# Kernel optimization log

Measured on AMD Instinct MI355X. Metric: run time of the kernel, lower is better.

## Reference

```python
import jax, jax.numpy as jnp
import numpy as np

NUM_SLOTS = 8
DIM = 256
N_HEADS = 4
ITERS = 5
HIDDEN = 512
EPS = 1e-8
DPH = DIM // N_HEADS
SCALE = DPH ** -0.5


def _ln(x, g, b):
    mu = x.mean(-1, keepdims=True)
    var = ((x - mu) ** 2).mean(-1, keepdims=True)
    return (x - mu) * jax.lax.rsqrt(var + 1e-5) * g + b


def setup_inputs() -> dict:
    key = jax.random.key(0)
    ks = jax.random.split(key, 12)
    B, N = 32, 4096
    def p(k, shape, s=0.02):
        return jax.random.normal(k, shape, jnp.float32) * s
    return {
        'inputs': jax.random.normal(ks[0], (B, N, DIM), jnp.float32),
        'slots_init': jax.random.normal(ks[1], (B, NUM_SLOTS, DIM), jnp.float32),
        'ln_f_g': jnp.ones(DIM, jnp.float32), 'ln_f_b': jnp.zeros(DIM, jnp.float32),
        'ln_s_g': jnp.ones(DIM, jnp.float32), 'ln_s_b': jnp.zeros(DIM, jnp.float32),
        'ln_ff_g': jnp.ones(DIM, jnp.float32), 'ln_ff_b': jnp.zeros(DIM, jnp.float32),
        'Wq': p(ks[2], (DIM, DIM)), 'bq': jnp.zeros(DIM, jnp.float32),
        'Wk': p(ks[3], (DIM, DIM)), 'bk': jnp.zeros(DIM, jnp.float32),
        'Wv': p(ks[4], (DIM, DIM)), 'bv': jnp.zeros(DIM, jnp.float32),
        'W_ih': p(ks[5], (3 * DIM, DIM)), 'b_ih': jnp.zeros(3 * DIM, jnp.float32),
        'W_hh': p(ks[6], (3 * DIM, DIM)), 'b_hh': jnp.zeros(3 * DIM, jnp.float32),
        'W1': p(ks[7], (DIM, HIDDEN)), 'b1': jnp.zeros(HIDDEN, jnp.float32),
        'W2': p(ks[8], (HIDDEN, DIM)), 'b2': jnp.zeros(DIM, jnp.float32),
    }


def reference(inputs, slots_init, ln_f_g, ln_f_b, ln_s_g, ln_s_b, ln_ff_g, ln_ff_b,
              Wq, bq, Wk, bk, Wv, bv, W_ih, b_ih, W_hh, b_hh, W1, b1, W2, b2):
    b, n, d = inputs.shape
    ns = slots_init.shape[1]
    x = _ln(inputs, ln_f_g, ln_f_b)                      # [b,n,d]
    k = (x @ Wk + bk).reshape(b, n, N_HEADS, DPH)
    v = (x @ Wv + bv).reshape(b, n, N_HEADS, DPH)
    slots = slots_init
    for _ in range(ITERS):
        slots_prev = slots
        s = _ln(slots, ln_s_g, ln_s_b)
        q = (s @ Wq + bq).reshape(b, ns, N_HEADS, DPH)
        dots = jnp.einsum('bihd,bjhd->bihj', q, k) * SCALE   # [b,ns,h,n]
        # softmax jointly over (slots, heads) per feature location j
        attn = jax.nn.softmax(dots.reshape(b, ns * N_HEADS, n), axis=1)
        attn = attn.reshape(b, ns, N_HEADS, n) + EPS
        attn = attn / attn.sum(-1, keepdims=True)
        updates = jnp.einsum('bjhd,bihj->bihd', v, attn).reshape(b, ns, d)
        # GRUCell (torch semantics): input=updates, hidden=slots_prev
        u = updates.reshape(-1, d)
        h = slots_prev.reshape(-1, d)
        gi = u @ W_ih.T + b_ih
        gh = h @ W_hh.T + b_hh
        ir, iz, inn = jnp.split(gi, 3, axis=-1)
        hr, hz, hnn = jnp.split(gh, 3, axis=-1)
        r = jax.nn.sigmoid(ir + hr)
        z = jax.nn.sigmoid(iz + hz)
        ng = jnp.tanh(inn + r * hnn)
        slots = ((1.0 - z) * ng + z * h).reshape(b, ns, d)
        # residual MLP
        slots = slots + (jax.nn.relu(_ln(slots, ln_ff_g, ln_ff_b) @ W1 + b1) @ W2 + b2)
    return slots
```

## Files before the change

### kernel.cpp

```cpp
#include <hip/hip_runtime.h>
#include <stdint.h>


#define NSLOT 8
#define R32   32
#define SEQN  4096

constexpr float EPSA    = 1e-8f;
constexpr float LNEPS   = 1e-5f;
constexpr float SCALE_F = 0.125f;

typedef short s16x8 __attribute__((ext_vector_type(8)));
typedef short s16x4 __attribute__((ext_vector_type(4)));
typedef float f32x4 __attribute__((ext_vector_type(4)));

__device__ __forceinline__ short f2bf(float f) {
  uint32_t u = __float_as_uint(f);
  uint32_t r = (u + 0x7FFFu + ((u >> 16) & 1u)) >> 16;
  return (short)r;
}
__device__ __forceinline__ s16x8 cvt8(const float* p) {
  f32x4 a = *(const f32x4*)p;
  f32x4 b = *(const f32x4*)(p + 4);
  s16x8 r;
  r[0]=f2bf(a[0]); r[1]=f2bf(a[1]); r[2]=f2bf(a[2]); r[3]=f2bf(a[3]);
  r[4]=f2bf(b[0]); r[5]=f2bf(b[1]); r[6]=f2bf(b[2]); r[7]=f2bf(b[3]);
  return r;
}

__global__ __launch_bounds__(256) void w_cast(
    const float* __restrict__ W_ih, const float* __restrict__ W_hh,
    const float* __restrict__ Wk,
    short* __restrict__ WihB, short* __restrict__ WhhB, short* __restrict__ WkB)
{
  int idx4 = blockIdx.x*256 + threadIdx.x;
  const float* src; short* dst; int off;
  if (idx4 < 49152)        { src = W_ih; dst = WihB; off = idx4; }
  else if (idx4 < 98304)   { src = W_hh; dst = WhhB; off = idx4 - 49152; }
  else                     { src = Wk;   dst = WkB;  off = idx4 - 98304; }
  f32x4 v = *(const f32x4*)(src + 4*(size_t)off);
  s16x4 o; o[0]=f2bf(v[0]); o[1]=f2bf(v[1]); o[2]=f2bf(v[2]); o[3]=f2bf(v[3]);
  *(s16x4*)(dst + 4*(size_t)off) = o;
}

__global__ __launch_bounds__(256) void w_trans(
    const float* __restrict__ Wv, const float* __restrict__ W1,
    const float* __restrict__ W2, const float* __restrict__ Wq,
    short* __restrict__ WvT, short* __restrict__ W1T,
    short* __restrict__ W2T, short* __restrict__ WqT)
{
  __shared__ float tile[64][65];
  int bid = blockIdx.x, t = threadIdx.x;
  const float* src; short* dst; int R, C, tr, tc;
  if (bid < 16)      { src = Wv; dst = WvT; R = 256; C = 256; int q = bid;      tr = q >> 2; tc = q & 3; }
  else if (bid < 48) { src = W1; dst = W1T; R = 256; C = 512; int q = bid - 16; tr = q >> 3; tc = q & 7; }
  else if (bid < 80) { src = W2; dst = W2T; R = 512; C = 256; int q = bid - 48; tr = q >> 2; tc = q & 3; }
  else               { src = Wq; dst = WqT; R = 256; C = 256; int q = bid - 80; tr = q >> 2; tc = q & 3; }
  int r0 = tr*64, c0 = tc*64;
  for (int p = t; p < 4096; p += 256) {
    int rr = p >> 6, cc = p & 63;
    tile[rr][cc] = src[(size_t)(r0 + rr)*C + c0 + cc];
  }
  __syncthreads();
  for (int p = t; p < 4096; p += 256) {
    int cc = p >> 6, rr = p & 63;
    dst[(size_t)(c0 + cc)*R + r0 + rr] = f2bf(tile[rr][cc]);
  }
}

__global__ __launch_bounds__(256) void s0_prep(
    const float* __restrict__ slots_init,
    const float* __restrict__ ln_s_g, const float* __restrict__ ln_s_b,
    const float* __restrict__ Wq, const float* __restrict__ bq,
    const float* __restrict__ Wk, const float* __restrict__ bk,
    float* __restrict__ slots_cur, short* __restrict__ qk, float* __restrict__ qb)
{
  __shared__ float red[8];
  __shared__ float sln[256], qv[256];
  int b = blockIdx.x >> 3, i = blockIdx.x & 7;
  int t = threadIdx.x;
  int row_base = (b*NSLOT + i)*256;
  float si = slots_init[row_base + t];
  slots_cur[row_base + t] = si;
  float s = si, s2 = si*si;
  #pragma unroll
  for (int m = 1; m < 64; m <<= 1) { s += __shfl_xor(s, m); s2 += __shfl_xor(s2, m); }
  if ((t & 63) == 0) { red[t >> 6] = s; red[4 + (t >> 6)] = s2; }
  __syncthreads();
  s  = red[0] + red[1] + red[2] + red[3];
  s2 = red[4] + red[5] + red[6] + red[7];
  float mu = s*(1.f/256.f), var = s2*(1.f/256.f) - mu*mu;
  float rs = 1.f/sqrtf(var + LNEPS);
  sln[t] = (si - mu)*rs*ln_s_g[t] + ln_s_b[t];
  __syncthreads();
  float acc = bq[t];
  for (int c = 0; c < 256; ++c) acc += sln[c]*Wq[(c << 8) + t];
  qv[t] = acc;
  __syncthreads();
  float a0 = 0.f, a1 = 0.f, a2 = 0.f, a3 = 0.f;
  const float* wr = Wk + ((size_t)t << 8);
  for (int d = 0; d < 64; ++d) {
    a0 += qv[d]*wr[d];         a1 += qv[64+d]*wr[64+d];
    a2 += qv[128+d]*wr[128+d]; a3 += qv[192+d]*wr[192+d];
  }
  short* qrow = qk + (size_t)(b*R32 + i*4)*256 + t;
  qrow[0]   = f2bf(SCALE_F*a0);
  qrow[256] = f2bf(SCALE_F*a1);
  qrow[512] = f2bf(SCALE_F*a2);
  qrow[768] = f2bf(SCALE_F*a3);
  int h = t >> 6, d2 = t & 63;
  float pv = qv[h*64 + d2]*bk[h*64 + d2];
  #pragma unroll
  for (int m = 1; m < 64; m <<= 1) pv += __shfl_xor(pv, m);
  if (d2 == 0) qb[b*R32 + i*4 + h] = SCALE_F*pv;
}

#define XSTR 264
#define TSTR 72
#define PSTR 72
#define OFF_XT   (64*XSTR*2)
#define OFF_PS   (OFF_XT + 256*TSTR*2)
#define OFF_PSUM (OFF_PS + 32*PSTR*2)
#define OFF_XSUM (OFF_PSUM + 4*32*4)
#define OFF_QB   (OFF_XSUM + 4*256*4)
#define SMEM_BYTES (OFF_QB + 32*4)

__global__ __launch_bounds__(256, 2) void attn_kernel(
    const float* __restrict__ inp,
    const float* __restrict__ ln_f_g, const float* __restrict__ ln_f_b,
    const short* __restrict__ qk, const float* __restrict__ qb,
    float* __restrict__ A_part, float* __restrict__ psum_part,
    float* __restrict__ xsum_part, int write_xsum)
{
  extern __shared__ char smem[];
  short* xs       = (short*)smem;
  short* xt       = (short*)(smem + OFF_XT);
  short* ps       = (short*)(smem + OFF_PS);
  float* psum_lds = (float*)(smem + OFF_PSUM);
  float* xsum_lds = (float*)(smem + OFF_XSUM);
  float* qb_lds   = (float*)(smem + OFF_QB);

  int tid = threadIdx.x;
  int w = tid >> 6, lane = tid & 63;
  int g = lane >> 4, lj = lane & 15;
  int b = blockIdx.x >> 4, chunk = blockIdx.x & 15;

  float gc[4], bc[4];
  #pragma unroll
  for (int q = 0; q < 4; ++q) { gc[q] = ln_f_g[lane + 64*q]; bc[q] = ln_f_b[lane + 64*q]; }

  if (tid < 32) qb_lds[tid] = qb[b*R32 + tid];

  s16x8 qkf[2][8];
  #pragma unroll
  for (int mt = 0; mt < 2; ++mt)
    #pragma unroll
    for (int ks = 0; ks < 8; ++ks)
      qkf[mt][ks] = *(const s16x8*)(qk + ((size_t)(b*R32 + mt*16 + lj) << 8) + ks*32 + g*8);
  __syncthreads();

  float qb0[4], qb1[4];
  #pragma unroll
  for (int r = 0; r < 4; ++r) { qb0[r] = qb_lds[4*g + r]; qb1[r] = qb_lds[16 + 4*g + r]; }

  f32x4 zero4 = {0.f, 0.f, 0.f, 0.f};
  f32x4 accD[2][4];
  #pragma unroll
  for (int mt = 0; mt < 2; ++mt)
    #pragma unroll
    for (int nt = 0; nt < 4; ++nt) accD[mt][nt] = zero4;
  float psum_acc[8] = {0.f,0.f,0.f,0.f,0.f,0.f,0.f,0.f};
  float xsum_acc[4] = {0.f,0.f,0.f,0.f};

  for (int step = 0; step < 4; ++step) {
    int jbase = chunk*256 + step*64;
    const float* rowp = inp + (((size_t)b*SEQN + jbase + w*16) << 8);
    short tq[4][4];
    #pragma unroll
    for (int rr = 0; rr < 16; ++rr) {
      const float* rp = rowp + ((size_t)rr << 8);
      float v0 = rp[lane], v1 = rp[lane+64], v2 = rp[lane+128], v3 = rp[lane+192];
      float s  = v0 + v1 + v2 + v3;
      float s2 = v0*v0 + v1*v1 + v2*v2 + v3*v3;
      #pragma unroll
      for (int m = 1; m < 64; m <<= 1) { s += __shfl_xor(s, m); s2 += __shfl_xor(s2, m); }
      float mu = s*(1.f/256.f);
      float var = s2*(1.f/256.f) - mu*mu;
      float rs = 1.f/sqrtf(var + LNEPS);
      int jrow = w*16 + rr;
      float vv[4] = {v0, v1, v2, v3};
      #pragma unroll
      for (int q = 0; q < 4; ++q) {
        float xl = (vv[q] - mu)*rs*gc[q] + bc[q];
        xsum_acc[q] += xl;
        short hv = f2bf(xl);
        xs[jrow*XSTR + lane + 64*q] = hv;
        tq[q][rr & 3] = hv;
      }
      if ((rr & 3) == 3) {
        #pragma unroll
        for (int q = 0; q < 4; ++q) {
          s16x4 pk = { tq[q][0], tq[q][1], tq[q][2], tq[q][3] };
          *(s16x4*)(xt + (lane + 64*q)*TSTR + w*16 + (rr - 3)) = pk;
        }
      }
    }
    f32x4 d0 = zero4, d1 = zero4;
    #pragma unroll
    for (int ks = 0; ks < 8; ++ks) {
      s16x8 bx = *(const s16x8*)(xs + (w*16 + lj)*XSTR + ks*32 + g*8);
      d0 = __builtin_amdgcn_mfma_f32_16x16x32_bf16(qkf[0][ks], bx, d0, 0, 0, 0);
      d1 = __builtin_amdgcn_mfma_f32_16x16x32_bf16(qkf[1][ks], bx, d1, 0, 0, 0);
    }
    {
      float m0 = -1e30f;
      #pragma unroll
      for (int r = 0; r < 4; ++r) {
        m0 = fmaxf(m0, d0[r] + qb0[r]);
        m0 = fmaxf(m0, d1[r] + qb1[r]);
      }
      m0 = fmaxf(m0, __shfl_xor(m0, 16));
      m0 = fmaxf(m0, __shfl_xor(m0, 32));
      float e0[4], e1[4], ssum = 0.f;
      #pragma unroll
      for (int r = 0; r < 4; ++r) {
        e0[r] = __expf(d0[r] + qb0[r] - m0);
        e1[r] = __expf(d1[r] + qb1[r] - m0);
        ssum += e0[r] + e1[r];
      }
      ssum += __shfl_xor(ssum, 16);
      ssum += __shfl_xor(ssum, 32);
      float inv = 1.f/ssum;
      int jl = w*16 + lj;
      #pragma unroll
      for (int r = 0; r < 4; ++r) {
        float sm0 = e0[r]*inv, sm1 = e1[r]*inv;
        psum_acc[r]     += sm0;
        psum_acc[4 + r] += sm1;
        ps[(4*g + r)*PSTR + jl]      = f2bf(sm0);
        ps[(16 + 4*g + r)*PSTR + jl] = f2bf(sm1);
      }
    }
    __syncthreads();
    #pragma unroll
    for (int ks = 0; ks < 2; ++ks) {
      s16x8 pa0 = *(const s16x8*)(ps + lj*PSTR + ks*32 + g*8);
      s16x8 pa1 = *(const s16x8*)(ps + (16 + lj)*PSTR + ks*32 + g*8);
      #pragma unroll
      for (int nt = 0; nt < 4; ++nt) {
        s16x8 bxt = *(const s16x8*)(xt + (w*64 + nt*16 + lj)*TSTR + ks*32 + g*8);
        accD[0][nt] = __builtin_amdgcn_mfma_f32_16x16x32_bf16(pa0, bxt, accD[0][nt], 0, 0, 0);
        accD[1][nt] = __builtin_amdgcn_mfma_f32_16x16x32_bf16(pa1, bxt, accD[1][nt], 0, 0, 0);
      }
    }
    __syncthreads();
  }

  {
    float* ap = A_part + ((size_t)(b*16 + chunk) << 13);
    #pragma unroll
    for (int mt = 0; mt < 2; ++mt)
      #pragma unroll
      for (int nt = 0; nt < 4; ++nt)
        #pragma unroll
        for (int r = 0; r < 4; ++r)
          ap[(mt*16 + 4*g + r)*256 + w*64 + nt*16 + lj] = accD[mt][nt][r];
  }
  #pragma unroll
  for (int r = 0; r < 8; ++r)
    #pragma unroll
    for (int m = 1; m < 16; m <<= 1) psum_acc[r] += __shfl_xor(psum_acc[r], m);
  if (lj == 0) {
    #pragma unroll
    for (int r = 0; r < 4; ++r) {
      psum_lds[w*32 + 4*g + r]      = psum_acc[r];
      psum_lds[w*32 + 16 + 4*g + r] = psum_acc[4 + r];
    }
  }
  #pragma unroll
  for (int q = 0; q < 4; ++q) xsum_lds[w*256 + lane + 64*q] = xsum_acc[q];
  __syncthreads();
  if (tid < 32) {
    float sv = psum_lds[tid] + psum_lds[32+tid] + psum_lds[64+tid] + psum_lds[96+tid];
    psum_part[(b*16 + chunk)*32 + tid] = sv;
  }
  if (write_xsum) {
    float sv = xsum_lds[tid] + xsum_lds[256+tid] + xsum_lds[512+tid] + xsum_lds[768+tid];
    xsum_part[((b*16 + chunk) << 8) + tid] = sv;
  }
}

#define AST 260
#define WST 520
#define S3_AF   0
#define S3_HP   (S3_AF + 32*AST)
#define S3_UU   (S3_HP + 8*AST)
#define S3_RZ   (S3_UU + 8*AST)
#define S3_INN  (S3_RZ + 8*WST)
#define S3_HNN  (S3_INN + 8*AST)
#define S3_SNL  (S3_HNN + 8*AST)
#define S3_LNS  (S3_SNL + 8*AST)
#define S3_HH   (S3_LNS + 8*AST)
#define S3_QV   (S3_HH + 8*WST)
#define S3_XSV  (S3_QV + 8*AST)
#define S3_SR   (S3_XSV + 256)
#define S3_BYTES ((S3_SR + 32)*4)

__global__ __launch_bounds__(256, 1) void s3_update(
    const float* __restrict__ A_part, const float* __restrict__ psum_part,
    const float* __restrict__ xsum_part,
    const short* __restrict__ WihB, const short* __restrict__ WhhB,
    const short* __restrict__ WkB,  const short* __restrict__ WvT,
    const short* __restrict__ W1T,  const short* __restrict__ W2T,
    const short* __restrict__ WqT,
    const float* __restrict__ bv,   const float* __restrict__ b_ih,
    const float* __restrict__ b_hh,
    const float* __restrict__ ln_ff_g, const float* __restrict__ ln_ff_b,
    const float* __restrict__ b1,   const float* __restrict__ b2,
    const float* __restrict__ ln_s_g, const float* __restrict__ ln_s_b,
    const float* __restrict__ bq,   const float* __restrict__ bk,
    float* __restrict__ slots_cur, short* __restrict__ qk,
    float* __restrict__ qb, float* __restrict__ out)
{
  extern __shared__ float sm[];
  int b = blockIdx.x, t = threadIdx.x;
  int w = t >> 6, lane = t & 63, g = lane >> 4, lj = lane & 15;
  int ar = lj & 7;

  {
    float x = 0.f;
    for (int ch = 0; ch < 16; ++ch) x += xsum_part[((b*16 + ch) << 8) + t];
    sm[S3_XSV + t] = x;
  }
  if (t < 32) {
    float p = 0.f;
    for (int ch = 0; ch < 16; ++ch) p += psum_part[(b*16 + ch)*32 + t];
    sm[S3_SR + t] = p + 4096.f*EPSA;
  }
  for (int idx = t; idx < 2048; idx += 256)
    sm[S3_HP + (idx >> 8)*AST + (idx & 255)] = slots_cur[b*2048 + idx];
  __syncthreads();
  for (int idx = t; idx < 8192; idx += 256) {
    int r = idx >> 8, c = idx & 255;
    float a = 0.f;
    for (int ch = 0; ch < 16; ++ch)
      a += A_part[(size_t)((b*16 + ch)*32 + r)*256 + c];
    sm[S3_AF + r*AST + c] = (a + EPSA*sm[S3_XSV + c]) / sm[S3_SR + r];
  }
  __syncthreads();

  {
    s16x8 af[8];
    const float* ab = sm + S3_AF + (ar*4 + w)*AST;
    #pragma unroll
    for (int ks = 0; ks < 8; ++ks) af[ks] = cvt8(ab + ks*32 + g*8);
    #pragma unroll
    for (int nt = 0; nt < 4; ++nt) {
      int n = w*64 + nt*16 + lj;
      f32x4 acc = {0.f,0.f,0.f,0.f};
      #pragma unroll
      for (int ks = 0; ks < 8; ++ks) {
        s16x8 bf = *(const s16x8*)(WvT + ((size_t)n << 8) + ks*32 + g*8);
        acc = __builtin_amdgcn_mfma_f32_16x16x32_bf16(af[ks], bf, acc, 0, 0, 0);
      }
      if (g < 2) {
        float bvn = bv[n];
        #pragma unroll
        for (int r = 0; r < 4; ++r) sm[S3_UU + (4*g + r)*AST + n] = acc[r] + bvn;
      }
    }
  }
  __syncthreads();

  {
    s16x8 uf[8], hf[8];
    const float* ub = sm + S3_UU + ar*AST;
    const float* hb = sm + S3_HP + ar*AST;
    #pragma unroll
    for (int ks = 0; ks < 8; ++ks) { uf[ks] = cvt8(ub + ks*32 + g*8); hf[ks] = cvt8(hb + ks*32 + g*8); }
    #pragma unroll
    for (int nt = 0; nt < 8; ++nt) {
      int n = w*128 + nt*16 + lj;
      f32x4 acc = {0.f,0.f,0.f,0.f};
      #pragma unroll
      for (int ks = 0; ks < 8; ++ks)
        acc = __builtin_amdgcn_mfma_f32_16x16x32_bf16(uf[ks], *(const s16x8*)(WihB + (size_t)n*256 + ks*32 + g*8), acc, 0, 0, 0);
      #pragma unroll
      for (int ks = 0; ks < 8; ++ks)
        acc = __builtin_amdgcn_mfma_f32_16x16x32_bf16(hf[ks], *(const s16x8*)(WhhB + (size_t)n*256 + ks*32 + g*8), acc, 0, 0, 0);
      if (g < 2) {
        float bb = b_ih[n] + b_hh[n];
        #pragma unroll
        for (int r = 0; r < 4; ++r) sm[S3_RZ + (4*g + r)*WST + n] = acc[r] + bb;
      }
    }
    #pragma unroll
    for (int nt = 0; nt < 4; ++nt) {
      int n = w*64 + nt*16 + lj;
      f32x4 ai = {0.f,0.f,0.f,0.f}, ah = {0.f,0.f,0.f,0.f};
      #pragma unroll
      for (int ks = 0; ks < 8; ++ks) {
        ai = __builtin_amdgcn_mfma_f32_16x16x32_bf16(uf[ks], *(const s16x8*)(WihB + (size_t)(512 + n)*256 + ks*32 + g*8), ai, 0, 0, 0);
        ah = __builtin_amdgcn_mfma_f32_16x16x32_bf16(hf[ks], *(const s16x8*)(WhhB + (size_t)(512 + n)*256 + ks*32 + g*8), ah, 0, 0, 0);
      }
      if (g < 2) {
        float bi2 = b_ih[512 + n], bh2 = b_hh[512 + n];
        #pragma unroll
        for (int r = 0; r < 4; ++r) {
          sm[S3_INN + (4*g + r)*AST + n] = ai[r] + bi2;
          sm[S3_HNN + (4*g + r)*AST + n] = ah[r] + bh2;
        }
      }
    }
  }
  __syncthreads();

  for (int idx = t; idx < 2048; idx += 256) {
    int s = idx >> 8, c = idx & 255;
    float rg = 1.f/(1.f + __expf(-sm[S3_RZ + s*WST + c]));
    float zg = 1.f/(1.f + __expf(-sm[S3_RZ + s*WST + 256 + c]));
    float ng = tanhf(sm[S3_INN + s*AST + c] + rg*sm[S3_HNN + s*AST + c]);
    sm[S3_SNL + s*AST + c] = (1.f - zg)*ng + zg*sm[S3_HP + s*AST + c];
  }
  __syncthreads();

  {
    int s = t >> 5, lg2 = t & 31;
    float s1 = 0.f, s2 = 0.f;
    for (int c = lg2; c < 256; c += 32) { float v = sm[S3_SNL + s*AST + c]; s1 += v; s2 += v*v; }
    #pragma unroll
    for (int m = 1; m < 32; m <<= 1) { s1 += __shfl_xor(s1, m); s2 += __shfl_xor(s2, m); }
    float mu = s1*(1.f/256.f), var = s2*(1.f/256.f) - mu*mu;
    float rs = 1.f/sqrtf(var + LNEPS);
    for (int c = lg2; c < 256; c += 32)
      sm[S3_LNS + s*AST + c] = (sm[S3_SNL + s*AST + c] - mu)*rs*ln_ff_g[c] + ln_ff_b[c];
  }
  __syncthreads();

  {
    s16x8 af[8];
    const float* ab = sm + S3_LNS + ar*AST;
    #pragma unroll
    for (int ks = 0; ks < 8; ++ks) af[ks] = cvt8(ab + ks*32 + g*8);
    #pragma unroll
    for (int nt = 0; nt < 8; ++nt) {
      int n = w*128 + nt*16 + lj;
      f32x4 acc = {0.f,0.f,0.f,0.f};
      #pragma unroll
      for (int ks = 0; ks < 8; ++ks)
        acc = __builtin_amdgcn_mfma_f32_16x16x32_bf16(af[ks], *(const s16x8*)(W1T + (size_t)n*256 + ks*32 + g*8), acc, 0, 0, 0);
      if (g < 2) {
        float b1n = b1[n];
        #pragma unroll
        for (int r = 0; r < 4; ++r) sm[S3_HH + (4*g + r)*WST + n] = fmaxf(acc[r] + b1n, 0.f);
      }
    }
  }
  __syncthreads();

  {
    s16x8 af[16];
    const float* ab = sm + S3_HH + ar*WST;
    #pragma unroll
    for (int ks = 0; ks < 16; ++ks) af[ks] = cvt8(ab + ks*32 + g*8);
    #pragma unroll
    for (int nt = 0; nt < 4; ++nt) {
      int n = w*64 + nt*16 + lj;
      f32x4 acc = {0.f,0.f,0.f,0.f};
      #pragma unroll
      for (int ks = 0; ks < 16; ++ks)
        acc = __builtin_amdgcn_mfma_f32_16x16x32_bf16(af[ks], *(const s16x8*)(W2T + (size_t)n*512 + ks*32 + g*8), acc, 0, 0, 0);
      if (g < 2) {
        float b2n = b2[n];
        #pragma unroll
        for (int r = 0; r < 4; ++r) {
          int s = 4*g + r;
          float sf = sm[S3_SNL + s*AST + n] + acc[r] + b2n;
          sm[S3_SNL + s*AST + n] = sf;
          out[(b*8 + s)*256 + n] = sf;
          slots_cur[(b*8 + s)*256 + n] = sf;
        }
      }
    }
  }
  __syncthreads();

  {
    int s = t >> 5, lg2 = t & 31;
    float s1 = 0.f, s2 = 0.f;
    for (int c = lg2; c < 256; c += 32) { float v = sm[S3_SNL + s*AST + c]; s1 += v; s2 += v*v; }
    #pragma unroll
    for (int m = 1; m < 32; m <<= 1) { s1 += __shfl_xor(s1, m); s2 += __shfl_xor(s2, m); }
    float mu = s1*(1.f/256.f), var = s2*(1.f/256.f) - mu*mu;
    float rs = 1.f/sqrtf(var + LNEPS);
    for (int c = lg2; c < 256; c += 32)
      sm[S3_LNS + s*AST + c] = (sm[S3_SNL + s*AST + c] - mu)*rs*ln_s_g[c] + ln_s_b[c];
  }
  __syncthreads();
  {
    s16x8 af[8];
    const float* ab = sm + S3_LNS + ar*AST;
    #pragma unroll
    for (int ks = 0; ks < 8; ++ks) af[ks] = cvt8(ab + ks*32 + g*8);
    #pragma unroll
    for (int nt = 0; nt < 4; ++nt) {
      int n = w*64 + nt*16 + lj;
      f32x4 acc = {0.f,0.f,0.f,0.f};
      #pragma unroll
      for (int ks = 0; ks < 8; ++ks)
        acc = __builtin_amdgcn_mfma_f32_16x16x32_bf16(af[ks], *(const s16x8*)(WqT + (size_t)n*256 + ks*32 + g*8), acc, 0, 0, 0);
      if (g < 2) {
        float bqn = bq[n];
        #pragma unroll
        for (int r = 0; r < 4; ++r) sm[S3_QV + (4*g + r)*AST + n] = acc[r] + bqn;
      }
    }
  }
  __syncthreads();

  {
    s16x8 af2[2];
    const float* ab = sm + S3_QV + ar*AST + w*64;
    af2[0] = cvt8(ab + g*8);
    af2[1] = cvt8(ab + 32 + g*8);
    #pragma unroll
    for (int nt = 0; nt < 16; ++nt) {
      int c = nt*16 + lj;
      f32x4 acc = {0.f,0.f,0.f,0.f};
      #pragma unroll
      for (int ks = 0; ks < 2; ++ks)
        acc = __builtin_amdgcn_mfma_f32_16x16x32_bf16(af2[ks], *(const s16x8*)(WkB + ((size_t)c << 8) + w*64 + ks*32 + g*8), acc, 0, 0, 0);
      if (g < 2) {
        #pragma unroll
        for (int r = 0; r < 4; ++r)
          qk[((size_t)b*R32 + (4*g + r)*4 + w)*256 + c] = f2bf(SCALE_F*acc[r]);
      }
    }
    int pr = t >> 3, dg = t & 7;
    int s = pr >> 2, h = pr & 3;
    float pv = 0.f;
    for (int d = dg*8; d < dg*8 + 8; ++d) pv += sm[S3_QV + s*AST + h*64 + d]*bk[h*64 + d];
    pv += __shfl_xor(pv, 1); pv += __shfl_xor(pv, 2); pv += __shfl_xor(pv, 4);
    if (dg == 0) qb[b*R32 + pr] = SCALE_F*pv;
  }
}

extern "C" void kernel_launch(void* const* d_in, const int* in_sizes, int n_in,
                              void* d_out, int out_size, void* d_ws, size_t ws_size,
                              hipStream_t stream) {
  (void)in_sizes; (void)n_in; (void)out_size; (void)ws_size;
  const float* inp        = (const float*)d_in[0];
  const float* slots_init = (const float*)d_in[1];
  const float* ln_f_g = (const float*)d_in[2];
  const float* ln_f_b = (const float*)d_in[3];
  const float* ln_s_g = (const float*)d_in[4];
  const float* ln_s_b = (const float*)d_in[5];
  const float* ln_ff_g = (const float*)d_in[6];
  const float* ln_ff_b = (const float*)d_in[7];
  const float* Wq = (const float*)d_in[8];
  const float* bq = (const float*)d_in[9];
  const float* Wk = (const float*)d_in[10];
  const float* bk = (const float*)d_in[11];
  const float* Wv = (const float*)d_in[12];
  const float* bv = (const float*)d_in[13];
  const float* W_ih = (const float*)d_in[14];
  const float* b_ih = (const float*)d_in[15];
  const float* W_hh = (const float*)d_in[16];
  const float* b_hh = (const float*)d_in[17];
  const float* W1 = (const float*)d_in[18];
  const float* b1 = (const float*)d_in[19];
  const float* W2 = (const float*)d_in[20];
  const float* b2 = (const float*)d_in[21];
  float* out = (float*)d_out;

  char* ws = (char*)d_ws;
  float* A_part    = (float*)(ws + 0);
  float* psum_part = (float*)(ws + 16777216);
  float* xsum_part = (float*)(ws + 16842752);
  short* qk        = (short*)(ws + 17367040);
  float* qbuf      = (float*)(ws + 17891328);
  float* slots_cur = (float*)(ws + 17895424);
  short* WihB      = (short*)(ws + 18157568);
  short* WhhB      = (short*)(ws + 18550784);
  short* WkB       = (short*)(ws + 18944000);
  short* WvT       = (short*)(ws + 19075072);
  short* W1T       = (short*)(ws + 19206144);
  short* W2T       = (short*)(ws + 19468288);
  short* WqT       = (short*)(ws + 19730432);

  hipFuncSetAttribute((const void*)attn_kernel,
                      hipFuncAttributeMaxDynamicSharedMemorySize, SMEM_BYTES);
  hipFuncSetAttribute((const void*)s3_update,
                      hipFuncAttributeMaxDynamicSharedMemorySize, S3_BYTES);

  w_cast<<<448, 256, 0, stream>>>(W_ih, W_hh, Wk, WihB, WhhB, WkB);
  w_trans<<<96, 256, 0, stream>>>(Wv, W1, W2, Wq, WvT, W1T, W2T, WqT);
  s0_prep<<<256, 256, 0, stream>>>(slots_init, ln_s_g, ln_s_b, Wq, bq, Wk, bk,
                                   slots_cur, qk, qbuf);
  for (int it = 0; it < 5; ++it) {
    attn_kernel<<<512, 256, SMEM_BYTES, stream>>>(inp, ln_f_g, ln_f_b, qk, qbuf,
                                                  A_part, psum_part, xsum_part,
                                                  it == 0 ? 1 : 0);
    s3_update<<<32, 256, S3_BYTES, stream>>>(A_part, psum_part, xsum_part,
                                             WihB, WhhB, WkB, WvT, W1T, W2T, WqT,
                                             bv, b_ih, b_hh, ln_ff_g, ln_ff_b,
                                             b1, b2, ln_s_g, ln_s_b, bq, bk,
                                             slots_cur, qk, qbuf, out);
  }
}
```

Measured before the change: 973.3 us.

## Precompute layernormed bf16 inputs once and split slot update across more blocks

Adds a prep kernel that layer-normalises the inputs once into bf16 row-major and transposed copies, so each of the five attention passes reads half-size bf16 data instead of recomputing LN from fp32. The slot update is split into a reduction kernel and a 128-block update kernel that uses scalar dot products instead of MFMA on 32 blocks. This path runs only when the workspace is large enough (about 156 MB). It costs 128 MB of extra scratch plus one extra write pass over the inputs.

```diff
diff --git a/kernel.cpp b/kernel.cpp
--- a/kernel.cpp
+++ b/kernel.cpp
@@ -19,13 +19,22 @@
   uint32_t r = (u + 0x7FFFu + ((u >> 16) & 1u)) >> 16;
   return (short)r;
 }
-__device__ __forceinline__ s16x8 cvt8(const float* p) {
-  f32x4 a = *(const f32x4*)p;
-  f32x4 b = *(const f32x4*)(p + 4);
-  s16x8 r;
-  r[0]=f2bf(a[0]); r[1]=f2bf(a[1]); r[2]=f2bf(a[2]); r[3]=f2bf(a[3]);
-  r[4]=f2bf(b[0]); r[5]=f2bf(b[1]); r[6]=f2bf(b[2]); r[7]=f2bf(b[3]);
-  return r;
+__device__ __forceinline__ float bf2f(short s) {
+  return __uint_as_float(((uint32_t)(uint16_t)s) << 16);
+}
+__device__ __forceinline__ float dotw(const short* __restrict__ w, const float* __restrict__ x, int n) {
+  float acc = 0.f;
+  #pragma unroll 4
+  for (int i = 0; i < n; i += 8) {
+    s16x8 wv = *(const s16x8*)(w + i);
+    f32x4 xa = *(const f32x4*)(x + i);
+    f32x4 xb = *(const f32x4*)(x + i + 4);
+    acc += bf2f(wv[0])*xa[0]; acc += bf2f(wv[1])*xa[1];
+    acc += bf2f(wv[2])*xa[2]; acc += bf2f(wv[3])*xa[3];
+    acc += bf2f(wv[4])*xb[0]; acc += bf2f(wv[5])*xb[1];
+    acc += bf2f(wv[6])*xb[2]; acc += bf2f(wv[7])*xb[3];
+  }
+  return acc;
 }
 
 __global__ __launch_bounds__(256) void w_cast(
@@ -115,6 +124,206 @@
   if (d2 == 0) qb[b*R32 + i*4 + h] = SCALE_F*pv;
 }
 
+__global__ __launch_bounds__(256) void xln_prep(
+    const float* __restrict__ inp,
+    const float* __restrict__ ln_f_g, const float* __restrict__ ln_f_b,
+    short* __restrict__ xln, short* __restrict__ xlnT, float* __restrict__ xsum64)
+{
+  __shared__ short ldsT[256*72];
+  __shared__ float xsred[4][256];
+  int b = blockIdx.x >> 6, jt = blockIdx.x & 63;
+  int t = threadIdx.x, w = t >> 6, lane = t & 63;
+  float gc[4], bc[4];
+  #pragma unroll
+  for (int q = 0; q < 4; ++q) { gc[q] = ln_f_g[lane + 64*q]; bc[q] = ln_f_b[lane + 64*q]; }
+  float xsum_acc[4] = {0.f,0.f,0.f,0.f};
+  #pragma unroll 4
+  for (int rr = 0; rr < 16; ++rr) {
+    int jl = w*16 + rr;
+    size_t row = ((size_t)b*SEQN + jt*64 + jl) << 8;
+    const float* rp = inp + row;
+    float v0 = rp[lane], v1 = rp[lane+64], v2 = rp[lane+128], v3 = rp[lane+192];
+    float s  = v0 + v1 + v2 + v3;
+    float s2 = v0*v0 + v1*v1 + v2*v2 + v3*v3;
+    #pragma unroll
+    for (int m = 1; m < 64; m <<= 1) { s += __shfl_xor(s, m); s2 += __shfl_xor(s2, m); }
+    float mu = s*(1.f/256.f), var = s2*(1.f/256.f) - mu*mu;
+    float rs = 1.f/sqrtf(var + LNEPS);
+    float vv[4] = {v0, v1, v2, v3};
+    #pragma unroll
+    for (int q = 0; q < 4; ++q) {
+      float xl = (vv[q] - mu)*rs*gc[q] + bc[q];
+      xsum_acc[q] += xl;
+      short hv = f2bf(xl);
+      xln[row + lane + 64*q] = hv;
+      int c = lane + 64*q;
+      ldsT[c*72 + (jl ^ (((c >> 3) & 7) << 3))] = hv;
+    }
+  }
+  #pragma unroll
+  for (int q = 0; q < 4; ++q) xsred[w][lane + 64*q] = xsum_acc[q];
+  __syncthreads();
+  xsum64[(((size_t)b*64 + jt) << 8) + t] =
+      xsred[0][t] + xsred[1][t] + xsred[2][t] + xsred[3][t];
+  #pragma unroll
+  for (int it = 0; it < 8; ++it) {
+    int cr = it*32 + (t >> 3);
+    int j0 = (t & 7)*8;
+    s16x8 v = *(const s16x8*)(ldsT + cr*72 + (j0 ^ (((cr >> 3) & 7) << 3)));
+    *(s16x8*)(xlnT + (((size_t)b*256 + cr) << 12) + jt*64 + j0) = v;
+  }
+}
+
+#define A2_XS   0
+#define A2_XT   (64*264*2)
+#define A2_PS   (A2_XT + 256*72*2)
+#define A2_PSUM (A2_PS + 32*72*2)
+#define A2_QB   (A2_PSUM + 128*4)
+#define A2_BYTES (A2_QB + 32*4)
+
+__global__ __launch_bounds__(256, 2) void attn2_kernel(
+    const short* __restrict__ xln, const short* __restrict__ xlnT,
+    const short* __restrict__ qk, const float* __restrict__ qb,
+    float* __restrict__ A_part, float* __restrict__ psum_part)
+{
+  extern __shared__ char smem[];
+  short* xs       = (short*)(smem + A2_XS);
+  short* xt       = (short*)(smem + A2_XT);
+  short* ps       = (short*)(smem + A2_PS);
+  float* psum_lds = (float*)(smem + A2_PSUM);
+  float* qb_lds   = (float*)(smem + A2_QB);
+
+  int tid = threadIdx.x;
+  int w = tid >> 6, lane = tid & 63;
+  int g = lane >> 4, lj = lane & 15;
+  int b = blockIdx.x >> 4, chunk = blockIdx.x & 15;
+  int xr3 = (lj & 3) << 3;
+
+  if (tid < 32) qb_lds[tid] = qb[b*R32 + tid];
+
+  s16x8 qkf[2][8];
+  #pragma unroll
+  for (int mt = 0; mt < 2; ++mt)
+    #pragma unroll
+    for (int ks = 0; ks < 8; ++ks)
+      qkf[mt][ks] = *(const s16x8*)(qk + ((size_t)(b*R32 + mt*16 + lj) << 8) + ks*32 + g*8);
+  __syncthreads();
+
+  float qb0[4], qb1[4];
+  #pragma unroll
+  for (int r = 0; r < 4; ++r) { qb0[r] = qb_lds[4*g + r]; qb1[r] = qb_lds[16 + 4*g + r]; }
+
+  f32x4 zero4 = {0.f, 0.f, 0.f, 0.f};
+  f32x4 accD[2][4];
+  #pragma unroll
+  for (int mt = 0; mt < 2; ++mt)
+    #pragma unroll
+    for (int nt = 0; nt < 4; ++nt) accD[mt][nt] = zero4;
+  float psum_acc[8] = {0.f,0.f,0.f,0.f,0.f,0.f,0.f,0.f};
+
+  for (int step = 0; step < 4; ++step) {
+    int jbase = chunk*256 + step*64;
+    const short* xrow = xln + (((size_t)b*SEQN + jbase) << 8);
+    #pragma unroll
+    for (int grp = 0; grp < 2; ++grp) {
+      int tr = w*16 + (grp*2 + (lane >> 5))*4;
+      int c0 = (lane & 31)*8;
+      s16x8 rv[4];
+      #pragma unroll
+      for (int k = 0; k < 4; ++k) rv[k] = *(const s16x8*)(xrow + ((size_t)(tr + k) << 8) + c0);
+      #pragma unroll
+      for (int k = 0; k < 4; ++k)
+        *(s16x8*)(xs + (tr + k)*264 + (c0 ^ (k << 3))) = rv[k];
+    }
+    const short* xtr = xlnT + (((size_t)b*256) << 12) + jbase;
+    #pragma unroll
+    for (int it = 0; it < 8; ++it) {
+      int cr = w*64 + it*8 + (lane >> 3);
+      int j0 = (lane & 7)*8;
+      s16x8 v = *(const s16x8*)(xtr + ((size_t)cr << 12) + j0);
+      *(s16x8*)(xt + cr*72 + (j0 ^ ((cr & 3) << 3))) = v;
+    }
+    f32x4 d0 = zero4, d1 = zero4;
+    #pragma unroll
+    for (int ks = 0; ks < 8; ++ks) {
+      s16x8 bx = *(const s16x8*)(xs + (w*16 + lj)*264 + ((ks*32 + g*8) ^ xr3));
+      d0 = __builtin_amdgcn_mfma_f32_16x16x32_bf16(qkf[0][ks], bx, d0, 0, 0, 0);
+      d1 = __builtin_amdgcn_mfma_f32_16x16x32_bf16(qkf[1][ks], bx, d1, 0, 0, 0);
+    }
+    {
+      float m0 = -1e30f;
+      #pragma unroll
+      for (int r = 0; r < 4; ++r) {
+        m0 = fmaxf(m0, d0[r] + qb0[r]);
+        m0 = fmaxf(m0, d1[r] + qb1[r]);
+      }
+      m0 = fmaxf(m0, __shfl_xor(m0, 16));
+      m0 = fmaxf(m0, __shfl_xor(m0, 32));
+      float e0[4], e1[4], ssum = 0.f;
+      #pragma unroll
+      for (int r = 0; r < 4; ++r) {
+        e0[r] = __expf(d0[r] + qb0[r] - m0);
+        e1[r] = __expf(d1[r] + qb1[r] - m0);
+        ssum += e0[r] + e1[r];
+      }
+      ssum += __shfl_xor(ssum, 16);
+      ssum += __shfl_xor(ssum, 32);
+      float inv = 1.f/ssum;
+      int jl = w*16 + lj;
+      #pragma unroll
+      for (int r = 0; r < 4; ++r) {
+        float sm0 = e0[r]*inv, sm1 = e1[r]*inv;
+        psum_acc[r]     += sm0;
+        psum_acc[4 + r] += sm1;
+        int jx = jl ^ (r << 3);
+        ps[(4*g + r)*72 + jx]      = f2bf(sm0);
+        ps[(16 + 4*g + r)*72 + jx] = f2bf(sm1);
+      }
+    }
+    __syncthreads();
+    #pragma unroll
+    for (int ks = 0; ks < 2; ++ks) {
+      int kx = (ks*32 + g*8) ^ xr3;
+      s16x8 pa0 = *(const s16x8*)(ps + lj*72 + kx);
+      s16x8 pa1 = *(const s16x8*)(ps + (16 + lj)*72 + kx);
+      #pragma unroll
+      for (int nt = 0; nt < 4; ++nt) {
+        s16x8 bxt = *(const s16x8*)(xt + (w*64 + nt*16 + lj)*72 + kx);
+        accD[0][nt] = __builtin_amdgcn_mfma_f32_16x16x32_bf16(pa0, bxt, accD[0][nt], 0, 0, 0);
+        accD[1][nt] = __builtin_amdgcn_mfma_f32_16x16x32_bf16(pa1, bxt, accD[1][nt], 0, 0, 0);
+      }
+    }
+    __syncthreads();
+  }
+
+  {
+    float* ap = A_part + ((size_t)(b*16 + chunk) << 13);
+    #pragma unroll
+    for (int mt = 0; mt < 2; ++mt)
+      #pragma unroll
+      for (int nt = 0; nt < 4; ++nt)
+        #pragma unroll
+        for (int r = 0; r < 4; ++r)
+          ap[(mt*16 + 4*g + r)*256 + w*64 + nt*16 + lj] = accD[mt][nt][r];
+  }
+  #pragma unroll
+  for (int r = 0; r < 8; ++r)
+    #pragma unroll
+    for (int m = 1; m < 16; m <<= 1) psum_acc[r] += __shfl_xor(psum_acc[r], m);
+  if (lj == 0) {
+    #pragma unroll
+    for (int r = 0; r < 4; ++r) {
+      psum_lds[w*32 + 4*g + r]      = psum_acc[r];
+      psum_lds[w*32 + 16 + 4*g + r] = psum_acc[4 + r];
+    }
+  }
+  __syncthreads();
+  if (tid < 32) {
+    float sv = psum_lds[tid] + psum_lds[32+tid] + psum_lds[64+tid] + psum_lds[96+tid];
+    psum_part[(b*16 + chunk)*32 + tid] = sv;
+  }
+}
+
 #define XSTR 264
 #define TSTR 72
 #define PSTR 72
@@ -290,25 +499,34 @@
   }
 }
 
-#define AST 260
-#define WST 520
-#define S3_AF   0
-#define S3_HP   (S3_AF + 32*AST)
-#define S3_UU   (S3_HP + 8*AST)
-#define S3_RZ   (S3_UU + 8*AST)
-#define S3_INN  (S3_RZ + 8*WST)
-#define S3_HNN  (S3_INN + 8*AST)
-#define S3_SNL  (S3_HNN + 8*AST)
-#define S3_LNS  (S3_SNL + 8*AST)
-#define S3_HH   (S3_LNS + 8*AST)
-#define S3_QV   (S3_HH + 8*WST)
-#define S3_XSV  (S3_QV + 8*AST)
-#define S3_SR   (S3_XSV + 256)
-#define S3_BYTES ((S3_SR + 32)*4)
-
-__global__ __launch_bounds__(256, 1) void s3_update(
+__global__ __launch_bounds__(256) void s3a_reduce(
     const float* __restrict__ A_part, const float* __restrict__ psum_part,
-    const float* __restrict__ xsum_part,
+    const float* __restrict__ xsum_part, int nchx, short* __restrict__ AfB)
+{
+  __shared__ float SrL[8];
+  int b = blockIdx.x >> 2, rg = blockIdx.x & 3;
+  int t = threadIdx.x;
+  if (t < 8) {
+    float p = 0.f;
+    for (int ch = 0; ch < 16; ++ch) p += psum_part[(b*16 + ch)*32 + rg*8 + t];
+    SrL[t] = p + 4096.f*EPSA;
+  }
+  float xsv = 0.f;
+  for (int ch = 0; ch < nchx; ++ch) xsv += xsum_part[(((size_t)b*nchx + ch) << 8) + t];
+  __syncthreads();
+  #pragma unroll 1
+  for (int k = 0; k < 8; ++k) {
+    int r = rg*8 + k;
+    float a = 0.f;
+    #pragma unroll
+    for (int ch = 0; ch < 16; ++ch)
+      a += A_part[((size_t)((b*16 + ch)*32 + r) << 8) + t];
+    AfB[((size_t)(b*32 + r) << 8) + t] = f2bf((a + EPSA*xsv) / SrL[k]);
+  }
+}
+
+__global__ __launch_bounds__(512) void s3b_update(
+    const short* __restrict__ AfB,
     const short* __restrict__ WihB, const short* __restrict__ WhhB,
     const short* __restrict__ WkB,  const short* __restrict__ WvT,
     const short* __restrict__ W1T,  const short* __restrict__ W2T,
@@ -322,233 +540,115 @@
     float* __restrict__ slots_cur, short* __restrict__ qk,
     float* __restrict__ qb, float* __restrict__ out)
 {
-  extern __shared__ float sm[];
-  int b = blockIdx.x, t = threadIdx.x;
-  int w = t >> 6, lane = t & 63, g = lane >> 4, lj = lane & 15;
-  int ar = lj & 7;
+  __shared__ float Af[2][4][256];
+  __shared__ float hp[2][256], uu[2][256], rz[2][512];
+  __shared__ float inn[2][256], hnn[2][256], snl[2][256], lns[2][256];
+  __shared__ float hhh[2][512], qv[2][256];
+  __shared__ float red[2][4][2];
+
+  int b = blockIdx.x >> 2, p = blockIdx.x & 3;
+  int t = threadIdx.x;
+  int sl = t >> 8, u = t & 255;
+  int si = p*2 + sl;
+  int row_base = (b*8 + si)*256;
+
+  #pragma unroll
+  for (int k = 0; k < 4; ++k)
+    Af[sl][k][u] = bf2f(AfB[((size_t)(b*32 + si*4 + k) << 8) + u]);
+  hp[sl][u] = slots_cur[row_base + u];
+  __syncthreads();
+
+  uu[sl][u] = bv[u] + dotw(WvT + ((size_t)u << 8), Af[sl][u >> 6], 256);
+  __syncthreads();
+
+  #pragma unroll
+  for (int rep = 0; rep < 2; ++rep) {
+    int n = rep*256 + u;
+    rz[sl][n] = b_ih[n] + b_hh[n]
+              + dotw(WihB + ((size_t)n << 8), uu[sl], 256)
+              + dotw(WhhB + ((size_t)n << 8), hp[sl], 256);
+  }
+  inn[sl][u] = b_ih[512 + u] + dotw(WihB + ((size_t)(512 + u) << 8), uu[sl], 256);
+  hnn[sl][u] = b_hh[512 + u] + dotw(WhhB + ((size_t)(512 + u) << 8), hp[sl], 256);
+  __syncthreads();
 
   {
-    float x = 0.f;
-    for (int ch = 0; ch < 16; ++ch) x += xsum_part[((b*16 + ch) << 8) + t];
-    sm[S3_XSV + t] = x;
-  }
-  if (t < 32) {
-    float p = 0.f;
-    for (int ch = 0; ch < 16; ++ch) p += psum_part[(b*16 + ch)*32 + t];
-    sm[S3_SR + t] = p + 4096.f*EPSA;
-  }
-  for (int idx = t; idx < 2048; idx += 256)
-    sm[S3_HP + (idx >> 8)*AST + (idx & 255)] = slots_cur[b*2048 + idx];
-  __syncthreads();
-  for (int idx = t; idx < 8192; idx += 256) {
-    int r = idx >> 8, c = idx & 255;
-    float a = 0.f;
-    for (int ch = 0; ch < 16; ++ch)
-      a += A_part[(size_t)((b*16 + ch)*32 + r)*256 + c];
-    sm[S3_AF + r*AST + c] = (a + EPSA*sm[S3_XSV + c]) / sm[S3_SR + r];
+    float rg = 1.f/(1.f + __expf(-rz[sl][u]));
+    float zg = 1.f/(1.f + __expf(-rz[sl][256 + u]));
+    float ng = tanhf(inn[sl][u] + rg*hnn[sl][u]);
+    snl[sl][u] = (1.f - zg)*ng + zg*hp[sl][u];
   }
   __syncthreads();
 
   {
-    s16x8 af[8];
-    const float* ab = sm + S3_AF + (ar*4 + w)*AST;
-    #pragma unroll
-    for (int ks = 0; ks < 8; ++ks) af[ks] = cvt8(ab + ks*32 + g*8);
-    #pragma unroll
-    for (int nt = 0; nt < 4; ++nt) {
-      int n = w*64 + nt*16 + lj;
-      f32x4 acc = {0.f,0.f,0.f,0.f};
-      #pragma unroll
-      for (int ks = 0; ks < 8; ++ks) {
-        s16x8 bf = *(const s16x8*)(WvT + ((size_t)n << 8) + ks*32 + g*8);
-        acc = __builtin_amdgcn_mfma_f32_16x16x32_bf16(af[ks], bf, acc, 0, 0, 0);
-      }
-      if (g < 2) {
-        float bvn = bv[n];
-        #pragma unroll
-        for (int r = 0; r < 4; ++r) sm[S3_UU + (4*g + r)*AST + n] = acc[r] + bvn;
-      }
-    }
+    float v = snl[sl][u];
+    float s = v, s2 = v*v;
+    #pragma unroll
+    for (int m = 1; m < 64; m <<= 1) { s += __shfl_xor(s, m); s2 += __shfl_xor(s2, m); }
+    int ww = (t >> 6) & 3;
+    if ((t & 63) == 0) { red[sl][ww][0] = s; red[sl][ww][1] = s2; }
+    __syncthreads();
+    s  = red[sl][0][0] + red[sl][1][0] + red[sl][2][0] + red[sl][3][0];
+    s2 = red[sl][0][1] + red[sl][1][1] + red[sl][2][1] + red[sl][3][1];
+    float mu = s*(1.f/256.f), var = s2*(1.f/256.f) - mu*mu;
+    float rs = 1.f/sqrtf(var + LNEPS);
+    lns[sl][u] = (snl[sl][u] - mu)*rs*ln_ff_g[u] + ln_ff_b[u];
+  }
+  __syncthreads();
+
+  #pragma unroll
+  for (int rep = 0; rep < 2; ++rep) {
+    int n = rep*256 + u;
+    hhh[sl][n] = fmaxf(b1[n] + dotw(W1T + ((size_t)n << 8), lns[sl], 256), 0.f);
   }
   __syncthreads();
 
   {
-    s16x8 uf[8], hf[8];
-    const float* ub = sm + S3_UU + ar*AST;
-    const float* hb = sm + S3_HP + ar*AST;
-    #pragma unroll
-    for (int ks = 0; ks < 8; ++ks) { uf[ks] = cvt8(ub + ks*32 + g*8); hf[ks] = cvt8(hb + ks*32 + g*8); }
-    #pragma unroll
-    for (int nt = 0; nt < 8; ++nt) {
-      int n = w*128 + nt*16 + lj;
-      f32x4 acc = {0.f,0.f,0.f,0.f};
-      #pragma unroll
-      for (int ks = 0; ks < 8; ++ks)
-        acc = __builtin_amdgcn_mfma_f32_16x16x32_bf16(uf[ks], *(const s16x8*)(WihB + (size_t)n*256 + ks*32 + g*8), acc, 0, 0, 0);
-      #pragma unroll
-      for (int ks = 0; ks < 8; ++ks)
-        acc = __builtin_amdgcn_mfma_f32_16x16x32_bf16(hf[ks], *(const s16x8*)(WhhB + (size_t)n*256 + ks*32 + g*8), acc, 0, 0, 0);
-      if (g < 2) {
-        float bb = b_ih[n] + b_hh[n];
-        #pragma unroll
-        for (int r = 0; r < 4; ++r) sm[S3_RZ + (4*g + r)*WST + n] = acc[r] + bb;
-      }
-    }
-    #pragma unroll
-    for (int nt = 0; nt < 4; ++nt) {
-      int n = w*64 + nt*16 + lj;
-      f32x4 ai = {0.f,0.f,0.f,0.f}, ah = {0.f,0.f,0.f,0.f};
-      #pragma unroll
-      for (int ks = 0; ks < 8; ++ks) {
-        ai = __builtin_amdgcn_mfma_f32_16x16x32_bf16(uf[ks], *(const s16x8*)(WihB + (size_t)(512 + n)*256 + ks*32 + g*8), ai, 0, 0, 0);
-        ah = __builtin_amdgcn_mfma_f32_16x16x32_bf16(hf[ks], *(const s16x8*)(WhhB + (size_t)(512 + n)*256 + ks*32 + g*8), ah, 0, 0, 0);
-      }
-      if (g < 2) {
-        float bi2 = b_ih[512 + n], bh2 = b_hh[512 + n];
-        #pragma unroll
-        for (int r = 0; r < 4; ++r) {
-          sm[S3_INN + (4*g + r)*AST + n] = ai[r] + bi2;
-          sm[S3_HNN + (4*g + r)*AST + n] = ah[r] + bh2;
-        }
-      }
-    }
-  }
-  __syncthreads();
-
-  for (int idx = t; idx < 2048; idx += 256) {
-    int s = idx >> 8, c = idx & 255;
-    float rg = 1.f/(1.f + __expf(-sm[S3_RZ + s*WST + c]));
-    float zg = 1.f/(1.f + __expf(-sm[S3_RZ + s*WST + 256 + c]));
-    float ng = tanhf(sm[S3_INN + s*AST + c] + rg*sm[S3_HNN + s*AST + c]);
-    sm[S3_SNL + s*AST + c] = (1.f - zg)*ng + zg*sm[S3_HP + s*AST + c];
+    float o = b2[u] + dotw(W2T + ((size_t)u << 9), hhh[sl], 512);
+    float sfin = snl[sl][u] + o;
+    snl[sl][u] = sfin;
+    out[row_base + u] = sfin;
+    slots_cur[row_base + u] = sfin;
   }
   __syncthreads();
 
   {
-    int s = t >> 5, lg2 = t & 31;
-    float s1 = 0.f, s2 = 0.f;
-    for (int c = lg2; c < 256; c += 32) { float v = sm[S3_SNL + s*AST + c]; s1 += v; s2 += v*v; }
-    #pragma unroll
-    for (int m = 1; m < 32; m <<= 1) { s1 += __shfl_xor(s1, m); s2 += __shfl_xor(s2, m); }
-    float mu = s1*(1.f/256.f), var = s2*(1.f/256.f) - mu*mu;
+    float v = snl[sl][u];
+    float s = v, s2 = v*v;
+    #pragma unroll
+    for (int m = 1; m < 64; m <<= 1) { s += __shfl_xor(s, m); s2 += __shfl_xor(s2, m); }
+    int ww = (t >> 6) & 3;
+    if ((t & 63) == 0) { red[sl][ww][0] = s; red[sl][ww][1] = s2; }
+    __syncthreads();
+    s  = red[sl][0][0] + red[sl][1][0] + red[sl][2][0] + red[sl][3][0];
+    s2 = red[sl][0][1] + red[sl][1][1] + red[sl][2][1] + red[sl][3][1];
+    float mu = s*(1.f/256.f), var = s2*(1.f/256.f) - mu*mu;
     float rs = 1.f/sqrtf(var + LNEPS);
-    for (int c = lg2; c < 256; c += 32)
-      sm[S3_LNS + s*AST + c] = (sm[S3_SNL + s*AST + c] - mu)*rs*ln_ff_g[c] + ln_ff_b[c];
-  }
-  __syncthreads();
-
-  {
-    s16x8 af[8];
-    const float* ab = sm + S3_LNS + ar*AST;
-    #pragma unroll
-    for (int ks = 0; ks < 8; ++ks) af[ks] = cvt8(ab + ks*32 + g*8);
-    #pragma unroll
-    for (int nt = 0; nt < 8; ++nt) {
-      int n = w*128 + nt*16 + lj;
-      f32x4 acc = {0.f,0.f,0.f,0.f};
-      #pragma unroll
-      for (int ks = 0; ks < 8; ++ks)
-        acc = __builtin_amdgcn_mfma_f32_16x16x32_bf16(af[ks], *(const s16x8*)(W1T + (size_t)n*256 + ks*32 + g*8), acc, 0, 0, 0);
-      if (g < 2) {
-        float b1n = b1[n];
-        #pragma unroll
-        for (int r = 0; r < 4; ++r) sm[S3_HH + (4*g + r)*WST + n] = fmaxf(acc[r] + b1n, 0.f);
-      }
-    }
-  }
-  __syncthreads();
-
-  {
-    s16x8 af[16];
-    const float* ab = sm + S3_HH + ar*WST;
-    #pragma unroll
-    for (int ks = 0; ks < 16; ++ks) af[ks] = cvt8(ab + ks*32 + g*8);
-    #pragma unroll
-    for (int nt = 0; nt < 4; ++nt) {
-      int n = w*64 + nt*16 + lj;
-      f32x4 acc = {0.f,0.f,0.f,0.f};
-      #pragma unroll
-      for (int ks = 0; ks < 16; ++ks)
-        acc = __builtin_amdgcn_mfma_f32_16x16x32_bf16(af[ks], *(const s16x8*)(W2T + (size_t)n*512 + ks*32 + g*8), acc, 0, 0, 0);
-      if (g < 2) {
-        float b2n = b2[n];
-        #pragma unroll
-        for (int r = 0; r < 4; ++r) {
-          int s = 4*g + r;
-          float sf = sm[S3_SNL + s*AST + n] + acc[r] + b2n;
-          sm[S3_SNL + s*AST + n] = sf;
-          out[(b*8 + s)*256 + n] = sf;
-          slots_cur[(b*8 + s)*256 + n] = sf;
-        }
-      }
-    }
-  }
-  __syncthreads();
-
-  {
-    int s = t >> 5, lg2 = t & 31;
-    float s1 = 0.f, s2 = 0.f;
-    for (int c = lg2; c < 256; c += 32) { float v = sm[S3_SNL + s*AST + c]; s1 += v; s2 += v*v; }
-    #pragma unroll
-    for (int m = 1; m < 32; m <<= 1) { s1 += __shfl_xor(s1, m); s2 += __shfl_xor(s2, m); }
-    float mu = s1*(1.f/256.f), var = s2*(1.f/256.f) - mu*mu;
-    float rs = 1.f/sqrtf(var + LNEPS);
-    for (int c = lg2; c < 256; c += 32)
-      sm[S3_LNS + s*AST + c] = (sm[S3_SNL + s*AST + c] - mu)*rs*ln_s_g[c] + ln_s_b[c];
-  }
-  __syncthreads();
-  {
-    s16x8 af[8];
-    const float* ab = sm + S3_LNS + ar*AST;
-    #pragma unroll
-    for (int ks = 0; ks < 8; ++ks) af[ks] = cvt8(ab + ks*32 + g*8);
-    #pragma unroll
-    for (int nt = 0; nt < 4; ++nt) {
-      int n = w*64 + nt*16 + lj;
-      f32x4 acc = {0.f,0.f,0.f,0.f};
-      #pragma unroll
-      for (int ks = 0; ks < 8; ++ks)
-        acc = __builtin_amdgcn_mfma_f32_16x16x32_bf16(af[ks], *(const s16x8*)(WqT + (size_t)n*256 + ks*32 + g*8), acc, 0, 0, 0);
-      if (g < 2) {
-        float bqn = bq[n];
-        #pragma unroll
-        for (int r = 0; r < 4; ++r) sm[S3_QV + (4*g + r)*AST + n] = acc[r] + bqn;
-      }
-    }
-  }
-  __syncthreads();
-
-  {
-    s16x8 af2[2];
-    const float* ab = sm + S3_QV + ar*AST + w*64;
-    af2[0] = cvt8(ab + g*8);
-    af2[1] = cvt8(ab + 32 + g*8);
-    #pragma unroll
-    for (int nt = 0; nt < 16; ++nt) {
-      int c = nt*16 + lj;
-      f32x4 acc = {0.f,0.f,0.f,0.f};
-      #pragma unroll
-      for (int ks = 0; ks < 2; ++ks)
-        acc = __builtin_amdgcn_mfma_f32_16x16x32_bf16(af2[ks], *(const s16x8*)(WkB + ((size_t)c << 8) + w*64 + ks*32 + g*8), acc, 0, 0, 0);
-      if (g < 2) {
-        #pragma unroll
-        for (int r = 0; r < 4; ++r)
-          qk[((size_t)b*R32 + (4*g + r)*4 + w)*256 + c] = f2bf(SCALE_F*acc[r]);
-      }
-    }
-    int pr = t >> 3, dg = t & 7;
-    int s = pr >> 2, h = pr & 3;
+    lns[sl][u] = (snl[sl][u] - mu)*rs*ln_s_g[u] + ln_s_b[u];
+  }
+  __syncthreads();
+  qv[sl][u] = bq[u] + dotw(WqT + ((size_t)u << 8), lns[sl], 256);
+  __syncthreads();
+
+  #pragma unroll
+  for (int h = 0; h < 4; ++h) {
+    float acc = dotw(WkB + ((size_t)u << 8) + h*64, &qv[sl][h*64], 64);
+    qk[((size_t)(b*R32 + si*4 + h) << 8) + u] = f2bf(SCALE_F*acc);
+  }
+  if (u < 32) {
+    int h = u >> 3, dg = u & 7;
     float pv = 0.f;
-    for (int d = dg*8; d < dg*8 + 8; ++d) pv += sm[S3_QV + s*AST + h*64 + d]*bk[h*64 + d];
+    #pragma unroll
+    for (int d = 0; d < 8; ++d) pv += qv[sl][h*64 + dg*8 + d]*bk[h*64 + dg*8 + d];
     pv += __shfl_xor(pv, 1); pv += __shfl_xor(pv, 2); pv += __shfl_xor(pv, 4);
-    if (dg == 0) qb[b*R32 + pr] = SCALE_F*pv;
+    if (dg == 0) qb[b*R32 + si*4 + h] = SCALE_F*pv;
   }
 }
 
 extern "C" void kernel_launch(void* const* d_in, const int* in_sizes, int n_in,
                               void* d_out, int out_size, void* d_ws, size_t ws_size,
                               hipStream_t stream) {
-  (void)in_sizes; (void)n_in; (void)out_size; (void)ws_size;
+  (void)in_sizes; (void)n_in; (void)out_size;
   const float* inp        = (const float*)d_in[0];
   const float* slots_init = (const float*)d_in[1];
   const float* ln_f_g = (const float*)d_in[2];
@@ -573,38 +673,59 @@
   const float* b2 = (const float*)d_in[21];
   float* out = (float*)d_out;
 
+  const size_t NEED_BIG = 156176384ULL;
+  bool big = ws_size >= NEED_BIG;
+  int nchx = big ? 64 : 16;
+
   char* ws = (char*)d_ws;
-  float* A_part    = (float*)(ws + 0);
-  float* psum_part = (float*)(ws + 16777216);
-  float* xsum_part = (float*)(ws + 16842752);
-  short* qk        = (short*)(ws + 17367040);
-  float* qbuf      = (float*)(ws + 17891328);
-  float* slots_cur = (float*)(ws + 17895424);
-  short* WihB      = (short*)(ws + 18157568);
-  short* WhhB      = (short*)(ws + 18550784);
-  short* WkB       = (short*)(ws + 18944000);
-  short* WvT       = (short*)(ws + 19075072);
-  short* W1T       = (short*)(ws + 19206144);
-  short* W2T       = (short*)(ws + 19468288);
-  short* WqT       = (short*)(ws + 19730432);
+  size_t o = 0;
+  auto alloc = [&](size_t bytes) { size_t r = o; o += (bytes + 255) & ~(size_t)255; return r; };
+  float* A_part    = (float*)(ws + alloc(16777216));
+  float* psum_part = (float*)(ws + alloc(65536));
+  float* xsum_part = (float*)(ws + alloc(big ? 2097152 : 524288));
+  short* qk        = (short*)(ws + alloc(524288));
+  float* qbuf      = (float*)(ws + alloc(4096));
+  float* slots_cur = (float*)(ws + alloc(262144));
+  short* AfB       = (short*)(ws + alloc(524288));
+  short* WihB      = (short*)(ws + alloc(393216));
+  short* WhhB      = (short*)(ws + alloc(393216));
+  short* WkB       = (short*)(ws + alloc(131072));
+  short* WvT       = (short*)(ws + alloc(131072));
+  short* W1T       = (short*)(ws + alloc(262144));
+  short* W2T       = (short*)(ws + alloc(262144));
+  short* WqT       = (short*)(ws + alloc(131072));
+  short* xln  = nullptr;
+  short* xlnT = nullptr;
+  if (big) {
+    xln  = (short*)(ws + alloc(67108864));
+    xlnT = (short*)(ws + alloc(67108864));
+  }
 
   hipFuncSetAttribute((const void*)attn_kernel,
                       hipFuncAttributeMaxDynamicSharedMemorySize, SMEM_BYTES);
-  hipFuncSetAttribute((const void*)s3_update,
-                      hipFuncAttributeMaxDynamicSharedMemorySize, S3_BYTES);
+  hipFuncSetAttribute((const void*)attn2_kernel,
+                      hipFuncAttributeMaxDynamicSharedMemorySize, A2_BYTES);
 
   w_cast<<<448, 256, 0, stream>>>(W_ih, W_hh, Wk, WihB, WhhB, WkB);
   w_trans<<<96, 256, 0, stream>>>(Wv, W1, W2, Wq, WvT, W1T, W2T, WqT);
   s0_prep<<<256, 256, 0, stream>>>(slots_init, ln_s_g, ln_s_b, Wq, bq, Wk, bk,
                                    slots_cur, qk, qbuf);
+  if (big) {
+    xln_prep<<<2048, 256, 0, stream>>>(inp, ln_f_g, ln_f_b, xln, xlnT, xsum_part);
+  }
   for (int it = 0; it < 5; ++it) {
-    attn_kernel<<<512, 256, SMEM_BYTES, stream>>>(inp, ln_f_g, ln_f_b, qk, qbuf,
-                                                  A_part, psum_part, xsum_part,
-                                                  it == 0 ? 1 : 0);
-    s3_update<<<32, 256, S3_BYTES, stream>>>(A_part, psum_part, xsum_part,
-                                             WihB, WhhB, WkB, WvT, W1T, W2T, WqT,
-                                             bv, b_ih, b_hh, ln_ff_g, ln_ff_b,
-                                             b1, b2, ln_s_g, ln_s_b, bq, bk,
-                                             slots_cur, qk, qbuf, out);
-  }
-}
+    if (big) {
+      attn2_kernel<<<512, 256, A2_BYTES, stream>>>(xln, xlnT, qk, qbuf,
+                                                   A_part, psum_part);
+    } else {
+      attn_kernel<<<512, 256, SMEM_BYTES, stream>>>(inp, ln_f_g, ln_f_b, qk, qbuf,
+                                                    A_part, psum_part, xsum_part,
+                                                    it == 0 ? 1 : 0);
+    }
+    s3a_reduce<<<128, 256, 0, stream>>>(A_part, psum_part, xsum_part, nchx, AfB);
+    s3b_update<<<128, 512, 0, stream>>>(AfB, WihB, WhhB, WkB, WvT, W1T, W2T, WqT,
+                                        bv, b_ih, b_hh, ln_ff_g, ln_ff_b,
+                                        b1, b2, ln_s_g, ln_s_b, bq, bk,
+                                        slots_cur, qk, qbuf, out);
+  }
+}
```

Result: slower. 1.079 ms (+10.8%).
